# Optimization experiments

Hardware: AMD Instinct MI355X
Metric: run time of the kernel (lower is better)

The kernel has to match this reference:

```python
import jax, jax.numpy as jnp
import numpy as np

D_IN = 1024
D_OUT = 1024
NUM_HEADS = 16
HEAD_DIM = D_OUT // NUM_HEADS


def setup_inputs() -> dict:
    key = jax.random.key(0)
    ks = jax.random.split(key, 9)
    s = 0.02
    return {
        "x": jax.random.normal(ks[0], (2, 2048, D_IN), dtype=jnp.float32),
        "Wq": jax.random.normal(ks[1], (D_IN, D_OUT), dtype=jnp.float32) * s,
        "bq": jnp.zeros((D_OUT,), dtype=jnp.float32),
        "Wk": jax.random.normal(ks[2], (D_IN, D_OUT), dtype=jnp.float32) * s,
        "bk": jnp.zeros((D_OUT,), dtype=jnp.float32),
        "Wv": jax.random.normal(ks[3], (D_IN, D_OUT), dtype=jnp.float32) * s,
        "bv": jnp.zeros((D_OUT,), dtype=jnp.float32),
        "Wo": jax.random.normal(ks[4], (D_OUT, D_OUT), dtype=jnp.float32) * s,
        "bo": jnp.zeros((D_OUT,), dtype=jnp.float32),
    }


def reference(x, Wq, bq, Wk, bk, Wv, bv, Wo, bo):
    B, S, _ = x.shape
    H, Dh = NUM_HEADS, HEAD_DIM
    q = (x @ Wq + bq).reshape(B, S, H, Dh).transpose(0, 2, 1, 3)  # bhsd
    k = (x @ Wk + bk).reshape(B, S, H, Dh).transpose(0, 2, 1, 3)
    v = (x @ Wv + bv).reshape(B, S, H, Dh).transpose(0, 2, 1, 3)
    scores = jnp.einsum("bhqd,bhkd->bhqk", q, k) * (Dh ** -0.5)
    causal = jnp.tril(jnp.ones((S, S), dtype=bool))
    scores = jnp.where(causal, scores, jnp.float32(-jnp.inf))
    w = jax.nn.softmax(scores, axis=-1)
    ctx = jnp.einsum("bhqk,bhkd->bhqd", w, v)
    ctx = ctx.transpose(0, 2, 1, 3).reshape(B, S, H * Dh)
    return ctx @ Wo + bo
```

## Files before the change

### kernel.cpp

```cpp
#include <hip/hip_runtime.h>
#include <cmath>

#define D_IN 1024
#define D_OUT 1024
#define NUM_HEADS 16
#define HEAD_DIM 64
#define BATCH 2
#define SEQ 2048
#define GK 1024
#define KT 32

typedef __attribute__((ext_vector_type(8))) short short8;
typedef __attribute__((ext_vector_type(4))) short short4v;
typedef __attribute__((ext_vector_type(4))) float float4v;

__device__ __forceinline__ unsigned short f2bf(float f) {
  unsigned int u = __builtin_bit_cast(unsigned int, f);
  unsigned int r = (u + 0x7FFFu + ((u >> 16) & 1u)) >> 16;
  return (unsigned short)r;
}

__device__ __forceinline__ void async_copy16(void* lds, const void* g) {
  __builtin_amdgcn_global_load_lds(
      (const __attribute__((address_space(1))) unsigned int*)g,
      (__attribute__((address_space(3))) unsigned int*)lds, 16, 0, 0);
}

#define DPP_F(x, ctrl) __builtin_bit_cast(float,                         \
    __builtin_amdgcn_update_dpp(__builtin_bit_cast(int, (x)),            \
                                __builtin_bit_cast(int, (x)),            \
                                (ctrl), 0xF, 0xF, false))

__device__ __forceinline__ float red16_sum(float x) {
  x += DPP_F(x, 0xB1);
  x += DPP_F(x, 0x4E);
  x += DPP_F(x, 0x124);
  x += DPP_F(x, 0x128);
  return x;
}

__global__ __launch_bounds__(256) void convert_x(const float* __restrict__ x,
                                                 unsigned short* __restrict__ xb) {
  const size_t i0 = ((size_t)blockIdx.x * 256 + threadIdx.x) * 8;
  float4 a = *(const float4*)(x + i0);
  float4 b = *(const float4*)(x + i0 + 4);
  union { unsigned short u[8]; short8 v; } t;
  t.u[0] = f2bf(a.x); t.u[1] = f2bf(a.y); t.u[2] = f2bf(a.z); t.u[3] = f2bf(a.w);
  t.u[4] = f2bf(b.x); t.u[5] = f2bf(b.y); t.u[6] = f2bf(b.z); t.u[7] = f2bf(b.w);
  *(short8*)(xb + i0) = t.v;
}

__global__ __launch_bounds__(256) void transpose_w(
    const float* __restrict__ Wq, const float* __restrict__ Wk,
    const float* __restrict__ Wv, const float* __restrict__ Wo,
    unsigned short* __restrict__ wqkv_t, unsigned short* __restrict__ wo_t) {
  const int z = blockIdx.z;
  const float* W = (z == 0) ? Wq : (z == 1) ? Wk : (z == 2) ? Wv : Wo;
  unsigned short* out = (z < 3) ? (wqkv_t + (size_t)z * 1024 * 1024) : wo_t;

  __shared__ float T[32][33];
  const int r = threadIdx.x >> 3;
  const int c4 = (threadIdx.x & 7) << 2;
  const int k0 = blockIdx.x * 32, n0 = blockIdx.y * 32;

  float4 v = *(const float4*)(W + (size_t)(k0 + r) * 1024 + n0 + c4);
  T[r][c4 + 0] = v.x; T[r][c4 + 1] = v.y; T[r][c4 + 2] = v.z; T[r][c4 + 3] = v.w;
  __syncthreads();

  union { unsigned short u[4]; short4v v4; } o;
#pragma unroll
  for (int i = 0; i < 4; ++i) o.u[i] = f2bf(T[c4 + i][r]);
  *(short4v*)(out + (size_t)(n0 + r) * 1024 + k0 + c4) = o.v4;
}

__device__ __forceinline__ void gemm_core(
    const unsigned short* __restrict__ A, const unsigned short* __restrict__ Bt,
    unsigned short* As, unsigned short* Bs, int bm, int bn, float4v acc[4][4]) {
  const int tid = threadIdx.x;
  const int wave = tid >> 6, lane = tid & 63;
  const int quad = lane >> 4, l16 = lane & 15;
  const int wr = wave >> 1, wc = wave & 1;
  const int sw = l16 & 7;

  int srow[4], sgc[4];
#pragma unroll
  for (int t = 0; t < 4; ++t) {
    const int c = (wave * 4 + t) * 64 + lane;
    srow[t] = c >> 3;
    sgc[t] = ((c & 7) ^ (srow[t] & 7)) * 8;
  }

  for (int k0 = 0; k0 < GK; k0 += 64) {
    __syncthreads();
#pragma unroll
    for (int t = 0; t < 4; ++t) {
      const int c = (wave * 4 + t) * 64 + lane;
      async_copy16(As + (size_t)c * 8, A + (size_t)(bm + srow[t]) * GK + k0 + sgc[t]);
    }
#pragma unroll
    for (int t = 0; t < 4; ++t) {
      const int c = (wave * 4 + t) * 64 + lane;
      async_copy16(Bs + (size_t)c * 8, Bt + (size_t)(bn + srow[t]) * GK + k0 + sgc[t]);
    }
    __syncthreads();

#pragma unroll
    for (int h = 0; h < 2; ++h) {
      short8 af[4], bf[4];
#pragma unroll
      for (int i = 0; i < 4; ++i) {
        const int row = wr * 64 + i * 16 + l16;
        af[i] = *(const short8*)&As[((size_t)row * 8 + ((h * 4 + quad) ^ sw)) * 8];
      }
#pragma unroll
      for (int j = 0; j < 4; ++j) {
        const int row = wc * 64 + j * 16 + l16;
        bf[j] = *(const short8*)&Bs[((size_t)row * 8 + ((h * 4 + quad) ^ sw)) * 8];
      }
#pragma unroll
      for (int i = 0; i < 4; ++i)
#pragma unroll
        for (int j = 0; j < 4; ++j)
          acc[i][j] = __builtin_amdgcn_mfma_f32_16x16x32_bf16(af[i], bf[j], acc[i][j], 0, 0, 0);
    }
  }
}

__global__ __launch_bounds__(256) void gemm_qkv(
    const unsigned short* __restrict__ A, const unsigned short* __restrict__ Bt,
    const float* __restrict__ bq, const float* __restrict__ bk,
    const float* __restrict__ bv,
    unsigned short* __restrict__ qbuf, unsigned short* __restrict__ kblk,
    unsigned short* __restrict__ vblk) {
  __shared__ unsigned short As[128 * 64];
  __shared__ unsigned short Bs[128 * 64];
  const int wave = threadIdx.x >> 6, lane = threadIdx.x & 63;
  const int quad = lane >> 4, l16 = lane & 15;
  const int wr = wave >> 1, wc = wave & 1;
  const int bm = blockIdx.x * 128, bn = blockIdx.y * 128;

  float4v acc[4][4] = {};
  gemm_core(A, Bt, As, Bs, bm, bn, acc);

#pragma unroll
  for (int j = 0; j < 4; ++j) {
    const int n = bn + wc * 64 + j * 16 + l16;
    const int seg = n >> 10, nn = n & 1023;
    const int h = nn >> 6, d = nn & 63;
    const float bsv = (seg == 0) ? bq[nn] : (seg == 1) ? bk[nn] : bv[nn];
    const float scale = (seg == 0) ? 0.18033688011112043f : 1.0f;
#pragma unroll
    for (int i = 0; i < 4; ++i) {
#pragma unroll
      for (int r = 0; r < 4; ++r) {
        const int m = bm + wr * 64 + i * 16 + quad * 4 + r;
        const int b = m >> 11, s = m & 2047;
        const int bh = b * NUM_HEADS + h;
        const unsigned short hv = f2bf((acc[i][j][r] + bsv) * scale);
        if (seg == 0) {
          qbuf[((size_t)bh * SEQ + s) * HEAD_DIM + d] = hv;
        } else if (seg == 1) {
          kblk[((size_t)bh * 64 + (s >> 5)) * 2048 +
               (size_t)(((((s >> 4) & 1) * 2 + (d >> 5)) * 64 +
                         ((d >> 3) & 3) * 16 + (s & 15)) * 8 + (d & 7))] = hv;
        } else {
          vblk[((size_t)bh * 64 + (s >> 5)) * 2048 +
               (size_t)(((d >> 4) * 64 + ((s >> 3) & 3) * 16 + (d & 15)) * 8 +
                        (s & 7))] = hv;
        }
      }
    }
  }
}

__global__ __launch_bounds__(256) void gemm_out(
    const unsigned short* __restrict__ A, const unsigned short* __restrict__ Bt,
    const float* __restrict__ bo, float* __restrict__ out) {
  __shared__ unsigned short As[128 * 64];
  __shared__ unsigned short Bs[128 * 64];
  const int wave = threadIdx.x >> 6, lane = threadIdx.x & 63;
  const int quad = lane >> 4, l16 = lane & 15;
  const int wr = wave >> 1, wc = wave & 1;
  const int bm = blockIdx.x * 128, bn = blockIdx.y * 128;

  float4v acc[4][4] = {};
  gemm_core(A, Bt, As, Bs, bm, bn, acc);

#pragma unroll
  for (int j = 0; j < 4; ++j) {
    const int n = bn + wc * 64 + j * 16 + l16;
    const float bsv = bo[n];
#pragma unroll
    for (int i = 0; i < 4; ++i) {
#pragma unroll
      for (int r = 0; r < 4; ++r) {
        const int m = bm + wr * 64 + i * 16 + quad * 4 + r;
        out[(size_t)m * D_OUT + n] = acc[i][j][r] + bsv;
      }
    }
  }
}

__global__ __launch_bounds__(64) void attn_kernel(
    const unsigned short* __restrict__ qf, const unsigned short* __restrict__ kblk,
    const unsigned short* __restrict__ vblk, unsigned short* __restrict__ partO,
    float* __restrict__ part_l) {
  __shared__ unsigned short PL[32 * 40];

  const int id = blockIdx.x;
  const int bh = id & 31;
  const int rest = id >> 5;
  const int sp = rest & 1;
  const int qblk = 63 - (rest >> 1);
  const int qw0 = qblk * 32;
  const int lane = threadIdx.x;
  const int quad = lane >> 4;
  const int l16 = lane & 15;

  const int nt = qblk + 1;
  const int t0 = sp ? (nt >> 1) : 0;
  const int t1 = sp ? nt : (nt >> 1);

  const size_t bh_base = (size_t)bh * SEQ * HEAD_DIM;
  const unsigned short* kb = kblk + bh_base;
  const unsigned short* vb = vblk + bh_base;

  short8 aq[2][2];
#pragma unroll
  for (int qt = 0; qt < 2; ++qt) {
    const unsigned short* qrow =
        qf + bh_base + (size_t)(qw0 + qt * 16 + l16) * HEAD_DIM + quad * 8;
    aq[qt][0] = *(const short8*)qrow;
    aq[qt][1] = *(const short8*)(qrow + 32);
  }

  float4v O[2][4] = {};
  float l_part[2][4] = {};

  if (t0 < t1) {
    short8 kA[4], vA[4], kB[4], vB[4];

    auto load = [&](int kt, short8 kd[4], short8 vd[4]) {
      const size_t base = (size_t)kt * 2048 + lane * 8;
#pragma unroll
      for (int f = 0; f < 4; ++f) kd[f] = *(const short8*)(kb + base + f * 512);
#pragma unroll
      for (int f = 0; f < 4; ++f) vd[f] = *(const short8*)(vb + base + f * 512);
    };

    auto step = [&](int kt, const short8 kd[4], const short8 vd[4], bool masked) {
      const int k0 = kt * KT;
      float4v cs[2][2];
#pragma unroll
      for (int qt = 0; qt < 2; ++qt)
#pragma unroll
        for (int g = 0; g < 2; ++g) {
          float4v c = {0.f, 0.f, 0.f, 0.f};
          c = __builtin_amdgcn_mfma_f32_16x16x32_bf16(aq[qt][0], kd[2 * g], c, 0, 0, 0);
          c = __builtin_amdgcn_mfma_f32_16x16x32_bf16(aq[qt][1], kd[2 * g + 1], c, 0, 0, 0);
          cs[qt][g] = c;
        }

#pragma unroll
      for (int qt = 0; qt < 2; ++qt)
#pragma unroll
        for (int g = 0; g < 2; ++g)
#pragma unroll
          for (int r = 0; r < 4; ++r) {
            float s = cs[qt][g][r];
            if (masked) {
              const int key = k0 + g * 16 + l16;
              const int qg = qw0 + qt * 16 + quad * 4 + r;
              s = (key <= qg) ? s : -1e30f;
            }
            const float p = __builtin_exp2f(s);
            l_part[qt][r] += p;
            const unsigned int pu = __builtin_bit_cast(unsigned int, p);
            PL[(qt * 16 + quad * 4 + r) * 40 + (g * 2 + (l16 >> 3)) * 8 + (l16 & 7)] =
                (unsigned short)(pu >> 16);
          }

#pragma unroll
      for (int qt = 0; qt < 2; ++qt) {
        const short8 pA = *(const short8*)&PL[(qt * 16 + l16) * 40 + quad * 8];
#pragma unroll
        for (int jj = 0; jj < 4; ++jj)
          O[qt][jj] = __builtin_amdgcn_mfma_f32_16x16x32_bf16(pA, vd[jj], O[qt][jj], 0, 0, 0);
      }
    };

    load(t0, kA, vA);
    int kt = t0;
    while (true) {
      const bool lastA = (kt == t1 - 1);
      if (!lastA) load(kt + 1, kB, vB);
      step(kt, kA, vA, kt == nt - 1);
      if (lastA) break;
      ++kt;
      const bool lastB = (kt == t1 - 1);
      if (!lastB) load(kt + 1, kA, vA);
      step(kt, kB, vB, kt == nt - 1);
      if (lastB) break;
      ++kt;
    }
  }

  const int u = (bh * 64 + qblk) * 2 + sp;
  unsigned short* po = partO + (size_t)u * 2048;
#pragma unroll
  for (int qt = 0; qt < 2; ++qt)
#pragma unroll
    for (int r = 0; r < 4; ++r) {
      const float lsum = red16_sum(l_part[qt][r]);
      const int row = qt * 16 + quad * 4 + r;
      if (l16 == 0) part_l[(size_t)u * 32 + row] = lsum;
#pragma unroll
      for (int jj = 0; jj < 4; ++jj)
        po[row * 64 + jj * 16 + l16] = f2bf(O[qt][jj][r]);
    }
}

__global__ __launch_bounds__(256) void combine_kernel(
    const unsigned short* __restrict__ partO, const float* __restrict__ part_l,
    unsigned short* __restrict__ ctx) {
  const int gid = blockIdx.x * 256 + threadIdx.x;
  const int d = (gid & 15) << 2;
  const int s = (gid >> 4) & 2047;
  const int bh = gid >> 15;
  const int qb = s >> 5, row = s & 31;

  const size_t base = (size_t)((bh * 64 + qb) * 2) * 2048 + row * 64 + d;
  const short4v p0 = *(const short4v*)(partO + base);
  const short4v p1 = *(const short4v*)(partO + base + 2048);
  const int lidx = (bh * 64 + qb) * 64 + row;
  const float inv = 1.0f / (part_l[lidx] + part_l[lidx + 32]);

  union { unsigned short u[4]; short4v v; } o;
#pragma unroll
  for (int i = 0; i < 4; ++i) {
    const float a = __builtin_bit_cast(float,
        (unsigned int)(unsigned short)p0[i] << 16);
    const float b = __builtin_bit_cast(float,
        (unsigned int)(unsigned short)p1[i] << 16);
    o.u[i] = f2bf((a + b) * inv);
  }
  const int bb = bh >> 4, h = bh & 15;
  *(short4v*)(ctx + ((size_t)bb * SEQ + s) * D_OUT + h * HEAD_DIM + d) = o.v;
}

extern "C" void kernel_launch(void* const* d_in, const int* in_sizes, int n_in,
                              void* d_out, int out_size, void* d_ws, size_t ws_size,
                              hipStream_t stream) {
  const float* x  = (const float*)d_in[0];
  const float* Wq = (const float*)d_in[1];
  const float* bq = (const float*)d_in[2];
  const float* Wk = (const float*)d_in[3];
  const float* bk = (const float*)d_in[4];
  const float* Wv = (const float*)d_in[5];
  const float* bv = (const float*)d_in[6];
  const float* Wo = (const float*)d_in[7];
  const float* bo = (const float*)d_in[8];
  float* out = (float*)d_out;

  const int M = BATCH * SEQ;
  unsigned short* xb     = (unsigned short*)d_ws;
  unsigned short* wqkv_t = xb + (size_t)M * D_IN;
  unsigned short* wo_t   = wqkv_t + (size_t)3 * D_OUT * D_IN;
  unsigned short* qb     = wo_t + (size_t)D_OUT * D_OUT;
  unsigned short* kblk   = qb + (size_t)M * D_OUT;
  unsigned short* vblk   = kblk + (size_t)M * D_OUT;
  unsigned short* cb     = vblk + (size_t)M * D_OUT;
  unsigned short* partO  = cb + (size_t)M * D_OUT;
  float*          part_l = (float*)(partO + (size_t)4096 * 2048);

  convert_x<<<(M * D_IN) / (256 * 8), 256, 0, stream>>>(x, xb);
  transpose_w<<<dim3(32, 32, 4), 256, 0, stream>>>(Wq, Wk, Wv, Wo, wqkv_t, wo_t);
  gemm_qkv<<<dim3(M / 128, 3 * D_OUT / 128), 256, 0, stream>>>(
      xb, wqkv_t, bq, bk, bv, qb, kblk, vblk);
  attn_kernel<<<dim3(32 * 64 * 2), 64, 0, stream>>>(qb, kblk, vblk, partO, part_l);
  combine_kernel<<<(32 * 2048 * 16) / 256, 256, 0, stream>>>(partO, part_l, cb);
  gemm_out<<<dim3(M / 128, D_OUT / 128), 256, 0, stream>>>(cb, wo_t, bo, out);
}
```

Baseline: 206.5 us.

## Split attention keys across four waves with in-block LDS combine; fuse prep kernels

The attention kernel now runs four waves per block. Each wave handles a quarter of the causal key range for one 32-row query block, and the partial outputs and row sums are reduced through shared memory inside the block. This removes the separate combine kernel and the global round-trip of partial outputs. The x conversion and weight transpose are merged into one prep launch to save a launch. The cost is more LDS per block, a block-wide barrier, and uneven per-wave work on short causal rows.

```diff
diff --git a/kernel.cpp b/kernel.cpp
--- a/kernel.cpp
+++ b/kernel.cpp
@@ -19,6 +19,9 @@
   unsigned int r = (u + 0x7FFFu + ((u >> 16) & 1u)) >> 16;
   return (unsigned short)r;
 }
+__device__ __forceinline__ float bf2f(unsigned short h) {
+  return __builtin_bit_cast(float, (unsigned int)h << 16);
+}
 
 __device__ __forceinline__ void async_copy16(void* lds, const void* g) {
   __builtin_amdgcn_global_load_lds(
@@ -39,22 +42,27 @@
   return x;
 }
 
-__global__ __launch_bounds__(256) void convert_x(const float* __restrict__ x,
-                                                 unsigned short* __restrict__ xb) {
-  const size_t i0 = ((size_t)blockIdx.x * 256 + threadIdx.x) * 8;
-  float4 a = *(const float4*)(x + i0);
-  float4 b = *(const float4*)(x + i0 + 4);
-  union { unsigned short u[8]; short8 v; } t;
-  t.u[0] = f2bf(a.x); t.u[1] = f2bf(a.y); t.u[2] = f2bf(a.z); t.u[3] = f2bf(a.w);
-  t.u[4] = f2bf(b.x); t.u[5] = f2bf(b.y); t.u[6] = f2bf(b.z); t.u[7] = f2bf(b.w);
-  *(short8*)(xb + i0) = t.v;
-}
-
-__global__ __launch_bounds__(256) void transpose_w(
-    const float* __restrict__ Wq, const float* __restrict__ Wk,
-    const float* __restrict__ Wv, const float* __restrict__ Wo,
+__global__ __launch_bounds__(256) void prep(
+    const float* __restrict__ x, const float* __restrict__ Wq,
+    const float* __restrict__ Wk, const float* __restrict__ Wv,
+    const float* __restrict__ Wo, unsigned short* __restrict__ xb,
     unsigned short* __restrict__ wqkv_t, unsigned short* __restrict__ wo_t) {
   const int z = blockIdx.z;
+  if (z == 4) {
+    const int bid = blockIdx.y * 32 + blockIdx.x;
+    const size_t i0 = ((size_t)bid * 256 + threadIdx.x) * 16;
+#pragma unroll
+    for (int half = 0; half < 2; ++half) {
+      const size_t o = i0 + half * 8;
+      float4 a = *(const float4*)(x + o);
+      float4 b = *(const float4*)(x + o + 4);
+      union { unsigned short u[8]; short8 v; } t;
+      t.u[0] = f2bf(a.x); t.u[1] = f2bf(a.y); t.u[2] = f2bf(a.z); t.u[3] = f2bf(a.w);
+      t.u[4] = f2bf(b.x); t.u[5] = f2bf(b.y); t.u[6] = f2bf(b.z); t.u[7] = f2bf(b.w);
+      *(short8*)(xb + o) = t.v;
+    }
+    return;
+  }
   const float* W = (z == 0) ? Wq : (z == 1) ? Wk : (z == 2) ? Wv : Wo;
   unsigned short* out = (z < 3) ? (wqkv_t + (size_t)z * 1024 * 1024) : wo_t;
 
@@ -201,25 +209,29 @@
   }
 }
 
-__global__ __launch_bounds__(64) void attn_kernel(
+#define OBS 72
+
+__global__ __launch_bounds__(256) void attn_kernel(
     const unsigned short* __restrict__ qf, const unsigned short* __restrict__ kblk,
-    const unsigned short* __restrict__ vblk, unsigned short* __restrict__ partO,
-    float* __restrict__ part_l) {
-  __shared__ unsigned short PL[32 * 40];
+    const unsigned short* __restrict__ vblk, unsigned short* __restrict__ ctx) {
+  __shared__ unsigned short PL[4 * 32 * 40];
+  __shared__ unsigned short OB[4 * 32 * OBS];
+  __shared__ float LL[4 * 32];
 
   const int id = blockIdx.x;
   const int bh = id & 31;
-  const int rest = id >> 5;
-  const int sp = rest & 1;
-  const int qblk = 63 - (rest >> 1);
+  const int qblk = 63 - (id >> 5);
   const int qw0 = qblk * 32;
-  const int lane = threadIdx.x;
+  const int tid = threadIdx.x;
+  const int w = tid >> 6;
+  const int lane = tid & 63;
   const int quad = lane >> 4;
   const int l16 = lane & 15;
 
   const int nt = qblk + 1;
-  const int t0 = sp ? (nt >> 1) : 0;
-  const int t1 = sp ? nt : (nt >> 1);
+  const int qch = (nt + 3) >> 2;
+  const int t0 = w * qch;
+  const int t1 = min(nt, t0 + qch);
 
   const size_t bh_base = (size_t)bh * SEQ * HEAD_DIM;
   const unsigned short* kb = kblk + bh_base;
@@ -236,6 +248,7 @@
 
   float4v O[2][4] = {};
   float l_part[2][4] = {};
+  unsigned short* PLw = PL + w * (32 * 40);
 
   if (t0 < t1) {
     short8 kA[4], vA[4], kB[4], vB[4];
@@ -276,13 +289,13 @@
             const float p = __builtin_exp2f(s);
             l_part[qt][r] += p;
             const unsigned int pu = __builtin_bit_cast(unsigned int, p);
-            PL[(qt * 16 + quad * 4 + r) * 40 + (g * 2 + (l16 >> 3)) * 8 + (l16 & 7)] =
+            PLw[(qt * 16 + quad * 4 + r) * 40 + (g * 2 + (l16 >> 3)) * 8 + (l16 & 7)] =
                 (unsigned short)(pu >> 16);
           }
 
 #pragma unroll
       for (int qt = 0; qt < 2; ++qt) {
-        const short8 pA = *(const short8*)&PL[(qt * 16 + l16) * 40 + quad * 8];
+        const short8 pA = *(const short8*)&PLw[(qt * 16 + l16) * 40 + quad * 8];
 #pragma unroll
         for (int jj = 0; jj < 4; ++jj)
           O[qt][jj] = __builtin_amdgcn_mfma_f32_16x16x32_bf16(pA, vd[jj], O[qt][jj], 0, 0, 0);
@@ -305,47 +318,36 @@
     }
   }
 
-  const int u = (bh * 64 + qblk) * 2 + sp;
-  unsigned short* po = partO + (size_t)u * 2048;
 #pragma unroll
   for (int qt = 0; qt < 2; ++qt)
 #pragma unroll
     for (int r = 0; r < 4; ++r) {
       const float lsum = red16_sum(l_part[qt][r]);
       const int row = qt * 16 + quad * 4 + r;
-      if (l16 == 0) part_l[(size_t)u * 32 + row] = lsum;
+      if (l16 == 0) LL[w * 32 + row] = lsum;
 #pragma unroll
       for (int jj = 0; jj < 4; ++jj)
-        po[row * 64 + jj * 16 + l16] = f2bf(O[qt][jj][r]);
-    }
-}
-
-__global__ __launch_bounds__(256) void combine_kernel(
-    const unsigned short* __restrict__ partO, const float* __restrict__ part_l,
-    unsigned short* __restrict__ ctx) {
-  const int gid = blockIdx.x * 256 + threadIdx.x;
-  const int d = (gid & 15) << 2;
-  const int s = (gid >> 4) & 2047;
-  const int bh = gid >> 15;
-  const int qb = s >> 5, row = s & 31;
-
-  const size_t base = (size_t)((bh * 64 + qb) * 2) * 2048 + row * 64 + d;
-  const short4v p0 = *(const short4v*)(partO + base);
-  const short4v p1 = *(const short4v*)(partO + base + 2048);
-  const int lidx = (bh * 64 + qb) * 64 + row;
-  const float inv = 1.0f / (part_l[lidx] + part_l[lidx + 32]);
-
-  union { unsigned short u[4]; short4v v; } o;
-#pragma unroll
-  for (int i = 0; i < 4; ++i) {
-    const float a = __builtin_bit_cast(float,
-        (unsigned int)(unsigned short)p0[i] << 16);
-    const float b = __builtin_bit_cast(float,
-        (unsigned int)(unsigned short)p1[i] << 16);
-    o.u[i] = f2bf((a + b) * inv);
-  }
-  const int bb = bh >> 4, h = bh & 15;
-  *(short4v*)(ctx + ((size_t)bb * SEQ + s) * D_OUT + h * HEAD_DIM + d) = o.v;
+        OB[(w * 32 + row) * OBS + jj * 16 + l16] = f2bf(O[qt][jj][r]);
+    }
+
+  __syncthreads();
+
+  const int row = w * 8 + (lane >> 3);
+  const int col0 = (lane & 7) * 8;
+  float acc[8] = {};
+#pragma unroll
+  for (int u = 0; u < 4; ++u) {
+    const short8 t = *(const short8*)&OB[(u * 32 + row) * OBS + col0];
+#pragma unroll
+    for (int i = 0; i < 8; ++i) acc[i] += bf2f((unsigned short)t[i]);
+  }
+  const float inv = 1.0f / (LL[row] + LL[32 + row] + LL[64 + row] + LL[96 + row]);
+  union { unsigned short u[8]; short8 v; } o;
+#pragma unroll
+  for (int i = 0; i < 8; ++i) o.u[i] = f2bf(acc[i] * inv);
+  const int b = bh >> 4, h = bh & 15;
+  const int qg = qw0 + row;
+  *(short8*)(ctx + ((size_t)b * SEQ + qg) * D_OUT + h * HEAD_DIM + col0) = o.v;
 }
 
 extern "C" void kernel_launch(void* const* d_in, const int* in_sizes, int n_in,
@@ -370,14 +372,10 @@
   unsigned short* kblk   = qb + (size_t)M * D_OUT;
   unsigned short* vblk   = kblk + (size_t)M * D_OUT;
   unsigned short* cb     = vblk + (size_t)M * D_OUT;
-  unsigned short* partO  = cb + (size_t)M * D_OUT;
-  float*          part_l = (float*)(partO + (size_t)4096 * 2048);
-
-  convert_x<<<(M * D_IN) / (256 * 8), 256, 0, stream>>>(x, xb);
-  transpose_w<<<dim3(32, 32, 4), 256, 0, stream>>>(Wq, Wk, Wv, Wo, wqkv_t, wo_t);
+
+  prep<<<dim3(32, 32, 5), 256, 0, stream>>>(x, Wq, Wk, Wv, Wo, xb, wqkv_t, wo_t);
   gemm_qkv<<<dim3(M / 128, 3 * D_OUT / 128), 256, 0, stream>>>(
       xb, wqkv_t, bq, bk, bv, qb, kblk, vblk);
-  attn_kernel<<<dim3(32 * 64 * 2), 64, 0, stream>>>(qb, kblk, vblk, partO, part_l);
-  combine_kernel<<<(32 * 2048 * 16) / 256, 256, 0, stream>>>(partO, part_l, cb);
+  attn_kernel<<<dim3(32 * 64), 256, 0, stream>>>(qb, kblk, vblk, cb);
   gemm_out<<<dim3(M / 128, D_OUT / 128), 256, 0, stream>>>(cb, wo_t, bo, out);
 }
```

New measurement: 205.5 us. About the same (-0.5%).
